# Kernel optimization log

Measured on AMD Instinct MI355X. Metric: run time of the kernel, lower is better.

Reference implementation:

```python
import jax, jax.numpy as jnp
import numpy as np

B, S, V = 4, 1024, 32000
TEMP = 1.0
EPS_LOW, EPS_HIGH = 0.2, 0.3


def setup_inputs() -> dict:
    key = jax.random.key(0)
    k1, k2, k3, k4 = jax.random.split(key, 4)
    logits = jax.random.normal(k1, (B, S, V), dtype=jnp.float32)
    input_ids = jax.random.randint(k2, (B, S), 0, V, dtype=jnp.int32)
    labels = jax.random.randint(k3, (B, S), 0, 2, dtype=jnp.int32)
    advantages = jax.random.normal(k4, (B,), dtype=jnp.float32)
    return {"logits": logits, "input_ids": input_ids, "labels": labels, "advantages": advantages}


def reference(logits, input_ids, labels, advantages):
    # shift: predict token t+1 from position t
    chosen_ids = input_ids[:, 1:]                      # [B, S-1]
    mask_loss = labels[:, 1:].astype(jnp.float32)      # [B, S-1]
    logits_for_loss = logits[:, :-1, :]                # [B, S-1, V]

    # per-token log-probs of chosen tokens (log_softmax then /temperature, as in source)
    logps_all = jax.nn.log_softmax(logits_for_loss, axis=-1)
    per_token_logps = jnp.take_along_axis(logps_all, chosen_ids[..., None], axis=-1)[..., 0] / TEMP

    # old policy logps (recomputed + stop_gradient path of the source)
    old_per_token_logps = jax.lax.stop_gradient(per_token_logps)

    # GRPO clipped per-token loss (what the Pallas kernel computes)
    ratio = jnp.exp(per_token_logps - old_per_token_logps)
    adv = advantages[:, None]                          # broadcast per sample
    unclipped = ratio * adv
    clipped = jnp.clip(ratio, 1.0 - EPS_LOW, 1.0 + EPS_HIGH) * adv
    per_token_loss = -jnp.minimum(unclipped, clipped)

    total_valid_token_count = mask_loss.sum()
    loss = (per_token_loss * mask_loss).sum() / total_valid_token_count

    # entropy pass over the full vocab (second sweep of the logits tensor)
    probs = jax.nn.softmax(logits_for_loss / TEMP, axis=-1)
    token_entropy = -jnp.sum(probs * jnp.log(probs + 1e-9), axis=-1)  # [B, S-1]
    masked_token_entropy = token_entropy * mask_loss
    avg_entropy_per_sample = masked_token_entropy.sum(axis=-1) / mask_loss.sum(axis=-1)

    # truncated entropy metric over valid tokens 4..100
    valid = mask_loss == 1
    cum_valid = jnp.cumsum(valid, axis=-1)
    entropy_calc_mask = jnp.logical_and(valid, jnp.logical_and(cum_valid >= 4, cum_valid <= 100))
    avg_entropy_truncated = (token_entropy * entropy_calc_mask).sum(axis=-1) / entropy_calc_mask.sum(axis=-1)

    return (loss,
            jax.lax.stop_gradient(per_token_logps),
            avg_entropy_per_sample,
            avg_entropy_truncated)
```

## Files before the change

kernel.cpp:

```cpp
#include <hip/hip_runtime.h>
#include <cmath>

#define NB 4
#define SEQ 1024
#define SM1 1023
#define VOC 32000
#define V4 (VOC / 4)

struct MST { float m, s, t; };

__device__ __forceinline__ MST mst_merge(MST a, MST b) {
    float M = fmaxf(a.m, b.m);
    float ca = __expf(a.m - M);
    float cb = __expf(b.m - M);
    MST r;
    r.m = M;
    r.s = fmaf(a.s, ca, b.s * cb);
    r.t = ca * fmaf(a.m - M, a.s, a.t) + cb * fmaf(b.m - M, b.s, b.t);
    return r;
}

__global__ __launch_bounds__(256) void k_rows(const float* __restrict__ logits,
                                              const int* __restrict__ input_ids,
                                              float* __restrict__ out,
                                              float* __restrict__ ent_ws) {
    const int s = blockIdx.x;
    const int b = blockIdx.y;
    const int tid = threadIdx.x;
    const size_t rowoff = (size_t)(b * SEQ + s) * VOC;
    const float4* __restrict__ row4 = (const float4*)(logits + rowoff);

    float m = -1e30f, S = 0.f, T = 0.f;
    for (int j = tid; j < V4; j += 256) {
        float4 x4 = row4[j];
        float xs[4] = {x4.x, x4.y, x4.z, x4.w};
        #pragma unroll
        for (int c = 0; c < 4; ++c) {
            float x = xs[c];
            if (x > m) {
                float cf = __expf(m - x);
                T = cf * fmaf(m - x, S, T);
                S = fmaf(S, cf, 1.0f);
                m = x;
            } else {
                float e = __expf(x - m);
                S += e;
                T = fmaf(e, x - m, T);
            }
        }
    }

    MST v{m, S, T};
    #pragma unroll
    for (int off = 32; off > 0; off >>= 1) {
        MST o;
        o.m = __shfl_xor(v.m, off);
        o.s = __shfl_xor(v.s, off);
        o.t = __shfl_xor(v.t, off);
        v = mst_merge(v, o);
    }

    __shared__ MST smst[4];
    const int lane = tid & 63, wid = tid >> 6;
    if (lane == 0) smst[wid] = v;
    __syncthreads();
    if (tid == 0) {
        MST r = smst[0];
        r = mst_merge(r, smst[1]);
        r = mst_merge(r, smst[2]);
        r = mst_merge(r, smst[3]);
        float logS = logf(r.s);
        int chosen = input_ids[b * SEQ + s + 1];
        float lc = logits[rowoff + (size_t)chosen];
        int row = b * SM1 + s;
        out[1 + row] = lc - r.m - logS;
        ent_ws[row] = logS - r.t / r.s;
    }
}

__global__ __launch_bounds__(1024) void k_persample(const int* __restrict__ labels,
                                                    const float* __restrict__ ent_ws,
                                                    float* __restrict__ out,
                                                    float* __restrict__ masksum_ws) {
    const int b = blockIdx.x;
    const int tid = threadIdx.x;
    const int lane = tid & 63, wid = tid >> 6;
    const bool has = tid < SM1;
    const int lab = has ? labels[b * SEQ + tid + 1] : 0;
    const float ent = has ? ent_ws[b * SM1 + tid] : 0.f;
    const int valid = (lab == 1) ? 1 : 0;

    int x = valid;
    #pragma unroll
    for (int off = 1; off < 64; off <<= 1) {
        int y = __shfl_up(x, off);
        if (lane >= off) x += y;
    }
    __shared__ int wsum[16];
    if (lane == 63) wsum[wid] = x;
    __syncthreads();
    if (tid == 0) {
        int acc = 0;
        #pragma unroll
        for (int i = 0; i < 16; ++i) { int t = wsum[i]; wsum[i] = acc; acc += t; }
    }
    __syncthreads();
    const int cum = x + wsum[wid];
    const int ecm = (valid && cum >= 4 && cum <= 100) ? 1 : 0;

    const float maskf = (float)valid;
    float4 acc;
    acc.x = maskf;
    acc.y = ent * maskf;
    acc.z = (float)ecm;
    acc.w = ent * (float)ecm;

    #pragma unroll
    for (int off = 32; off > 0; off >>= 1) {
        acc.x += __shfl_xor(acc.x, off);
        acc.y += __shfl_xor(acc.y, off);
        acc.z += __shfl_xor(acc.z, off);
        acc.w += __shfl_xor(acc.w, off);
    }
    __shared__ float4 wacc[16];
    if (lane == 0) wacc[wid] = acc;
    __syncthreads();
    if (tid == 0) {
        float4 t = wacc[0];
        #pragma unroll
        for (int i = 1; i < 16; ++i) {
            t.x += wacc[i].x; t.y += wacc[i].y; t.z += wacc[i].z; t.w += wacc[i].w;
        }
        out[1 + NB * SM1 + b]      = t.y / t.x;
        out[1 + NB * SM1 + NB + b] = t.w / t.z;
        masksum_ws[b] = t.x;
    }
}

__global__ void k_loss(const float* __restrict__ adv,
                       const float* __restrict__ masksum_ws,
                       float* __restrict__ out) {
    if (threadIdx.x == 0 && blockIdx.x == 0) {
        float tot = 0.f, num = 0.f;
        #pragma unroll
        for (int b = 0; b < NB; ++b) {
            float ms = masksum_ws[b];
            tot += ms;
            num = fmaf(adv[b], ms, num);
        }
        out[0] = -num / tot;
    }
}

extern "C" void kernel_launch(void* const* d_in, const int* in_sizes, int n_in,
                              void* d_out, int out_size, void* d_ws, size_t ws_size,
                              hipStream_t stream) {
    const float* logits    = (const float*)d_in[0];
    const int*   input_ids = (const int*)d_in[1];
    const int*   labels    = (const int*)d_in[2];
    const float* adv       = (const float*)d_in[3];
    float* out = (float*)d_out;
    float* ent_ws = (float*)d_ws;
    float* masksum_ws = ent_ws + NB * SM1;

    k_rows<<<dim3(SM1, NB), 256, 0, stream>>>(logits, input_ids, out, ent_ws);
    k_persample<<<NB, 1024, 0, stream>>>(labels, ent_ws, out, masksum_ws);
    k_loss<<<1, 64, 0, stream>>>(adv, masksum_ws, out);
}
```

Before: 101.6 us.

## Use dual accumulators with nontemporal loads and merge tail kernels into one

The row kernel now keeps two independent online softmax/entropy accumulators fed by two nontemporal float4 loads per iteration, which adds memory-level parallelism and breaks the serial dependency chain. The chosen-token gather is issued before the sweep by thread 0, so its latency overlaps the main loop. The per-sample and loss kernels are fused into one single-block kernel that loops over the batch, saving one launch at the cost of serialising the four samples in a single block.

```diff
diff --git a/kernel.cpp b/kernel.cpp
--- a/kernel.cpp
+++ b/kernel.cpp
@@ -6,6 +6,8 @@
 #define SM1 1023
 #define VOC 32000
 #define V4 (VOC / 4)
+
+typedef float f4 __attribute__((ext_vector_type(4)));
 
 struct MST { float m, s, t; };
 
@@ -20,6 +22,19 @@
     return r;
 }
 
+__device__ __forceinline__ void upd(float x, float& m, float& S, float& T) {
+    if (x > m) {
+        float cf = __expf(m - x);
+        T = cf * fmaf(m - x, S, T);
+        S = fmaf(S, cf, 1.0f);
+        m = x;
+    } else {
+        float e = __expf(x - m);
+        S += e;
+        T = fmaf(e, x - m, T);
+    }
+}
+
 __global__ __launch_bounds__(256) void k_rows(const float* __restrict__ logits,
                                               const int* __restrict__ input_ids,
                                               float* __restrict__ out,
@@ -28,29 +43,33 @@
     const int b = blockIdx.y;
     const int tid = threadIdx.x;
     const size_t rowoff = (size_t)(b * SEQ + s) * VOC;
-    const float4* __restrict__ row4 = (const float4*)(logits + rowoff);
+    const f4* __restrict__ row4 = (const f4*)(logits + rowoff);
 
-    float m = -1e30f, S = 0.f, T = 0.f;
-    for (int j = tid; j < V4; j += 256) {
-        float4 x4 = row4[j];
-        float xs[4] = {x4.x, x4.y, x4.z, x4.w};
-        #pragma unroll
-        for (int c = 0; c < 4; ++c) {
-            float x = xs[c];
-            if (x > m) {
-                float cf = __expf(m - x);
-                T = cf * fmaf(m - x, S, T);
-                S = fmaf(S, cf, 1.0f);
-                m = x;
-            } else {
-                float e = __expf(x - m);
-                S += e;
-                T = fmaf(e, x - m, T);
-            }
-        }
+    float lc = 0.f;
+    if (tid == 0) {
+        int chosen = input_ids[b * SEQ + s + 1];
+        lc = logits[rowoff + (size_t)chosen];
     }
 
-    MST v{m, S, T};
+    float m0 = -1e30f, S0 = 0.f, T0 = 0.f;
+    float m1 = -1e30f, S1 = 0.f, T1 = 0.f;
+
+    int j = tid;
+    for (; j + 256 < V4; j += 512) {
+        f4 xa = __builtin_nontemporal_load(row4 + j);
+        f4 xb = __builtin_nontemporal_load(row4 + j + 256);
+        upd(xa.x, m0, S0, T0); upd(xa.y, m0, S0, T0);
+        upd(xa.z, m0, S0, T0); upd(xa.w, m0, S0, T0);
+        upd(xb.x, m1, S1, T1); upd(xb.y, m1, S1, T1);
+        upd(xb.z, m1, S1, T1); upd(xb.w, m1, S1, T1);
+    }
+    if (j < V4) {
+        f4 xa = __builtin_nontemporal_load(row4 + j);
+        upd(xa.x, m0, S0, T0); upd(xa.y, m0, S0, T0);
+        upd(xa.z, m0, S0, T0); upd(xa.w, m0, S0, T0);
+    }
+
+    MST v = mst_merge(MST{m0, S0, T0}, MST{m1, S1, T1});
     #pragma unroll
     for (int off = 32; off > 0; off >>= 1) {
         MST o;
@@ -70,83 +89,76 @@
         r = mst_merge(r, smst[2]);
         r = mst_merge(r, smst[3]);
         float logS = logf(r.s);
-        int chosen = input_ids[b * SEQ + s + 1];
-        float lc = logits[rowoff + (size_t)chosen];
         int row = b * SM1 + s;
         out[1 + row] = lc - r.m - logS;
         ent_ws[row] = logS - r.t / r.s;
     }
 }
 
-__global__ __launch_bounds__(1024) void k_persample(const int* __restrict__ labels,
-                                                    const float* __restrict__ ent_ws,
-                                                    float* __restrict__ out,
-                                                    float* __restrict__ masksum_ws) {
-    const int b = blockIdx.x;
+__global__ __launch_bounds__(1024) void k_tail(const int* __restrict__ labels,
+                                               const float* __restrict__ ent_ws,
+                                               const float* __restrict__ adv,
+                                               float* __restrict__ out) {
     const int tid = threadIdx.x;
     const int lane = tid & 63, wid = tid >> 6;
-    const bool has = tid < SM1;
-    const int lab = has ? labels[b * SEQ + tid + 1] : 0;
-    const float ent = has ? ent_ws[b * SM1 + tid] : 0.f;
-    const int valid = (lab == 1) ? 1 : 0;
+    __shared__ int wsum[16];
+    __shared__ float4 wacc[16];
+    __shared__ float msum[NB];
 
-    int x = valid;
-    #pragma unroll
-    for (int off = 1; off < 64; off <<= 1) {
-        int y = __shfl_up(x, off);
-        if (lane >= off) x += y;
+    for (int b = 0; b < NB; ++b) {
+        const bool has = tid < SM1;
+        const int lab = has ? labels[b * SEQ + tid + 1] : 0;
+        const float ent = has ? ent_ws[b * SM1 + tid] : 0.f;
+        const int valid = (lab == 1) ? 1 : 0;
+
+        int x = valid;
+        #pragma unroll
+        for (int off = 1; off < 64; off <<= 1) {
+            int y = __shfl_up(x, off);
+            if (lane >= off) x += y;
+        }
+        if (lane == 63) wsum[wid] = x;
+        __syncthreads();
+        int woff = 0;
+        #pragma unroll
+        for (int i = 0; i < 16; ++i) woff += (i < wid) ? wsum[i] : 0;
+        const int cum = woff + x;
+        const int ecm = (valid && cum >= 4 && cum <= 100) ? 1 : 0;
+
+        float4 acc;
+        acc.x = (float)valid;
+        acc.y = ent * (float)valid;
+        acc.z = (float)ecm;
+        acc.w = ent * (float)ecm;
+        #pragma unroll
+        for (int off = 32; off > 0; off >>= 1) {
+            acc.x += __shfl_xor(acc.x, off);
+            acc.y += __shfl_xor(acc.y, off);
+            acc.z += __shfl_xor(acc.z, off);
+            acc.w += __shfl_xor(acc.w, off);
+        }
+        if (lane == 0) wacc[wid] = acc;
+        __syncthreads();
+        if (tid == 0) {
+            float4 t = wacc[0];
+            #pragma unroll
+            for (int i = 1; i < 16; ++i) {
+                t.x += wacc[i].x; t.y += wacc[i].y;
+                t.z += wacc[i].z; t.w += wacc[i].w;
+            }
+            out[1 + NB * SM1 + b]      = t.y / t.x;
+            out[1 + NB * SM1 + NB + b] = t.w / t.z;
+            msum[b] = t.x;
+        }
+        __syncthreads();
     }
-    __shared__ int wsum[16];
-    if (lane == 63) wsum[wid] = x;
-    __syncthreads();
+
     if (tid == 0) {
-        int acc = 0;
-        #pragma unroll
-        for (int i = 0; i < 16; ++i) { int t = wsum[i]; wsum[i] = acc; acc += t; }
-    }
-    __syncthreads();
-    const int cum = x + wsum[wid];
-    const int ecm = (valid && cum >= 4 && cum <= 100) ? 1 : 0;
-
-    const float maskf = (float)valid;
-    float4 acc;
-    acc.x = maskf;
-    acc.y = ent * maskf;
-    acc.z = (float)ecm;
-    acc.w = ent * (float)ecm;
-
-    #pragma unroll
-    for (int off = 32; off > 0; off >>= 1) {
-        acc.x += __shfl_xor(acc.x, off);
-        acc.y += __shfl_xor(acc.y, off);
-        acc.z += __shfl_xor(acc.z, off);
-        acc.w += __shfl_xor(acc.w, off);
-    }
-    __shared__ float4 wacc[16];
-    if (lane == 0) wacc[wid] = acc;
-    __syncthreads();
-    if (tid == 0) {
-        float4 t = wacc[0];
-        #pragma unroll
-        for (int i = 1; i < 16; ++i) {
-            t.x += wacc[i].x; t.y += wacc[i].y; t.z += wacc[i].z; t.w += wacc[i].w;
-        }
-        out[1 + NB * SM1 + b]      = t.y / t.x;
-        out[1 + NB * SM1 + NB + b] = t.w / t.z;
-        masksum_ws[b] = t.x;
-    }
-}
-
-__global__ void k_loss(const float* __restrict__ adv,
-                       const float* __restrict__ masksum_ws,
-                       float* __restrict__ out) {
-    if (threadIdx.x == 0 && blockIdx.x == 0) {
         float tot = 0.f, num = 0.f;
         #pragma unroll
         for (int b = 0; b < NB; ++b) {
-            float ms = masksum_ws[b];
-            tot += ms;
-            num = fmaf(adv[b], ms, num);
+            tot += msum[b];
+            num = fmaf(adv[b], msum[b], num);
         }
         out[0] = -num / tot;
     }
@@ -161,9 +173,7 @@
     const float* adv       = (const float*)d_in[3];
     float* out = (float*)d_out;
     float* ent_ws = (float*)d_ws;
-    float* masksum_ws = ent_ws + NB * SM1;
 
     k_rows<<<dim3(SM1, NB), 256, 0, stream>>>(logits, input_ids, out, ent_ws);
-    k_persample<<<NB, 1024, 0, stream>>>(labels, ent_ws, out, masksum_ws);
-    k_loss<<<1, 64, 0, stream>>>(adv, masksum_ws, out);
+    k_tail<<<1, 1024, 0, stream>>>(labels, ent_ws, adv, out);
 }
```

After: 95.30 us. 6.2% less time.
